# Kernel tuning notes

Hardware: AMD Instinct MI355X
Metric: run time of the kernel (lower is better)

The kernel has to match this reference:

```python
import jax, jax.numpy as jnp
import numpy as np

HID = 768  # hidden_size; feature dim is 2*HID


def setup_inputs() -> dict:
    key = jax.random.key(0)
    k1, k2 = jax.random.split(key)
    B, N, K, total_Q, D = 4, 10, 5, 512, 2 * HID
    support = jax.random.normal(k1, (B, N, K, D), dtype=jnp.float32)
    query = jax.random.normal(k2, (B, total_Q, D), dtype=jnp.float32)
    return {"support": support, "query": query, "N": N, "K": K, "total_Q": total_Q}


def reference(support, query, N, K, total_Q):
    B = support.shape[0]
    D = support.shape[-1]
    # (B, N*K, D)
    S = support.reshape(B, N * K, D)
    # negative squared euclidean distance: broadcast (B,1,NK,D) vs (B,Q,1,D) -> (B,Q,NK)
    dist_sq = -jnp.sum((S[:, None, :, :] - query[:, :, None, :]) ** 2, axis=3)
    dist_sq = dist_sq.reshape(B, total_Q, N, K)
    # query-guided weights: mean over queries, tanh, softmax over K -> (B,N,K,1)
    qgw = jax.nn.softmax(jnp.tanh(jnp.mean(dist_sq, axis=1)), axis=-1)[..., None]
    # weighted aggregation over shots -> (B,N,D)
    agg = jnp.sum(support * qgw, axis=2)
    return agg, qgw
```

## Files before the change

### kernel.cpp

```cpp
#include <hip/hip_runtime.h>
#include <math.h>

constexpr int B = 4;
constexpr int N = 10;
constexpr int K = 5;
constexpr int Q = 512;
constexpr int D = 1536;

constexpr int QBAR_OFF = 0;
constexpr int CSUM_OFF = B * D;

__global__ __launch_bounds__(256) void qstats_kernel(
    const float* __restrict__ query, float* __restrict__ ws) {
    const int tid = threadIdx.x;
    const int d   = blockIdx.y * 256 + tid;
    const int b   = blockIdx.z;
    const int q0  = blockIdx.x * 64;

    const float* qp = query + (size_t)b * Q * D + (size_t)q0 * D + d;
    float acc = 0.f, ssq = 0.f;
#pragma unroll 8
    for (int q = 0; q < 64; ++q) {
        float v = qp[(size_t)q * D];
        acc += v;
        ssq = fmaf(v, v, ssq);
    }
    atomicAdd(&ws[QBAR_OFF + b * D + d], acc);

    for (int off = 32; off > 0; off >>= 1) ssq += __shfl_down(ssq, off);
    __shared__ float red[4];
    const int wave = tid >> 6, lane = tid & 63;
    if (lane == 0) red[wave] = ssq;
    __syncthreads();
    if (tid == 0) {
        atomicAdd(&ws[CSUM_OFF + b], red[0] + red[1] + red[2] + red[3]);
    }
}

__global__ __launch_bounds__(256) void agg_kernel(
    const float* __restrict__ support, const float* __restrict__ ws,
    float* __restrict__ out) {
    const int tid = threadIdx.x;
    const int bn  = blockIdx.x;
    const int b   = bn / N;

    const float* sup  = support + (size_t)bn * K * D;
    const float* qbar = ws + QBAR_OFF + (size_t)b * D;

    __shared__ float s_red[2][K][4];
    __shared__ float s_w[K];

    const int wave = tid >> 6, lane = tid & 63;

    for (int k = 0; k < K; ++k) {
        float a = 0.f, c = 0.f;
        for (int d = tid; d < D; d += 256) {
            float s = sup[k * D + d];
            a = fmaf(s, s, a);
            c = fmaf(s, qbar[d], c);
        }
        for (int off = 32; off > 0; off >>= 1) {
            a += __shfl_down(a, off);
            c += __shfl_down(c, off);
        }
        if (lane == 0) { s_red[0][k][wave] = a; s_red[1][k][wave] = c; }
    }
    __syncthreads();

    if (tid < K) {
        const int k = tid;
        float ssk = s_red[0][k][0] + s_red[0][k][1] + s_red[0][k][2] + s_red[0][k][3];
        float sqk = s_red[1][k][0] + s_red[1][k][1] + s_red[1][k][2] + s_red[1][k][3];
        float cb  = ws[CSUM_OFF + b] * (1.f / Q);
        float m = -ssk + 2.f * sqk * (1.f / Q) - cb;
        s_w[k] = tanhf(m);
    }
    __syncthreads();
    if (tid == 0) {
        float mx = s_w[0];
        for (int k = 1; k < K; ++k) mx = fmaxf(mx, s_w[k]);
        float e[K], sum = 0.f;
        for (int k = 0; k < K; ++k) { e[k] = expf(s_w[k] - mx); sum += e[k]; }
        float inv = 1.f / sum;
        for (int k = 0; k < K; ++k) s_w[k] = e[k] * inv;
    }
    __syncthreads();

    if (tid < K) out[(size_t)B * N * D + bn * K + tid] = s_w[tid];

    float w[K];
#pragma unroll
    for (int k = 0; k < K; ++k) w[k] = s_w[k];

    for (int d = tid; d < D; d += 256) {
        float acc = 0.f;
#pragma unroll
        for (int k = 0; k < K; ++k) acc = fmaf(sup[k * D + d], w[k], acc);
        out[(size_t)bn * D + d] = acc;
    }
}

extern "C" void kernel_launch(void* const* d_in, const int* in_sizes, int n_in,
                              void* d_out, int out_size, void* d_ws, size_t ws_size,
                              hipStream_t stream) {
    const float* support = (const float*)d_in[0];
    const float* query   = (const float*)d_in[1];
    float* out = (float*)d_out;
    float* ws  = (float*)d_ws;

    hipMemsetAsync(d_ws, 0, (size_t)(B * D + B) * sizeof(float), stream);

    dim3 g1(Q / 64, D / 256, B);
    qstats_kernel<<<g1, 256, 0, stream>>>(query, ws);

    agg_kernel<<<B * N, 256, 0, stream>>>(support, ws, out);
}
```

Measured before the change: 86.51 us.

## Replace atomics and memset with partial-sum workspace reduced in agg kernel

The query-statistics kernel now writes per-chunk partial sums to distinct workspace slots instead of issuing atomicAdds. The aggregation kernel reduces those partials into shared memory (qbar and the squared-norm constant) before computing the weights. This removes the hipMemsetAsync launch and atomic contention, and the shared qbar also serves the dot-product loop. In exchange, each of the 40 agg blocks redundantly sums 8 partial rows of D floats.

```diff
diff --git a/kernel.cpp b/kernel.cpp
--- a/kernel.cpp
+++ b/kernel.cpp
@@ -7,17 +7,21 @@
 constexpr int Q = 512;
 constexpr int D = 1536;
 
-constexpr int QBAR_OFF = 0;
-constexpr int CSUM_OFF = B * D;
+constexpr int QCH = 8;
+constexpr int DCH = 6;
+
+constexpr int PART_OFF = 0;
+constexpr int CS_OFF   = QCH * B * D;
 
 __global__ __launch_bounds__(256) void qstats_kernel(
     const float* __restrict__ query, float* __restrict__ ws) {
     const int tid = threadIdx.x;
-    const int d   = blockIdx.y * 256 + tid;
+    const int c   = blockIdx.x;
+    const int y   = blockIdx.y;
     const int b   = blockIdx.z;
-    const int q0  = blockIdx.x * 64;
+    const int d   = y * 256 + tid;
 
-    const float* qp = query + (size_t)b * Q * D + (size_t)q0 * D + d;
+    const float* qp = query + (size_t)b * Q * D + (size_t)(c * 64) * D + d;
     float acc = 0.f, ssq = 0.f;
 #pragma unroll 8
     for (int q = 0; q < 64; ++q) {
@@ -25,7 +29,7 @@
         acc += v;
         ssq = fmaf(v, v, ssq);
     }
-    atomicAdd(&ws[QBAR_OFF + b * D + d], acc);
+    ws[PART_OFF + ((size_t)c * B + b) * D + d] = acc;
 
     for (int off = 32; off > 0; off >>= 1) ssq += __shfl_down(ssq, off);
     __shared__ float red[4];
@@ -33,7 +37,7 @@
     if (lane == 0) red[wave] = ssq;
     __syncthreads();
     if (tid == 0) {
-        atomicAdd(&ws[CSUM_OFF + b], red[0] + red[1] + red[2] + red[3]);
+        ws[CS_OFF + (b * QCH + c) * DCH + y] = red[0] + red[1] + red[2] + red[3];
     }
 }
 
@@ -44,26 +48,39 @@
     const int bn  = blockIdx.x;
     const int b   = bn / N;
 
-    const float* sup  = support + (size_t)bn * K * D;
-    const float* qbar = ws + QBAR_OFF + (size_t)b * D;
+    const float* sup = support + (size_t)bn * K * D;
 
+    __shared__ float s_qbar[D];
     __shared__ float s_red[2][K][4];
-    __shared__ float s_w[K];
+    __shared__ float s_w[K + 1];
+
+    for (int d = tid; d < D; d += 256) {
+        float s = 0.f;
+#pragma unroll
+        for (int c = 0; c < QCH; ++c)
+            s += ws[PART_OFF + ((size_t)c * B + b) * D + d];
+        s_qbar[d] = s;
+    }
+    if (tid < 64) {
+        float v = (tid < QCH * DCH) ? ws[CS_OFF + b * (QCH * DCH) + tid] : 0.f;
+        for (int off = 32; off > 0; off >>= 1) v += __shfl_down(v, off);
+        if (tid == 0) s_w[K] = v * (1.f / Q);
+    }
+    __syncthreads();
 
     const int wave = tid >> 6, lane = tid & 63;
-
     for (int k = 0; k < K; ++k) {
-        float a = 0.f, c = 0.f;
+        float a = 0.f, cdot = 0.f;
         for (int d = tid; d < D; d += 256) {
             float s = sup[k * D + d];
-            a = fmaf(s, s, a);
-            c = fmaf(s, qbar[d], c);
+            a    = fmaf(s, s, a);
+            cdot = fmaf(s, s_qbar[d], cdot);
         }
         for (int off = 32; off > 0; off >>= 1) {
-            a += __shfl_down(a, off);
-            c += __shfl_down(c, off);
+            a    += __shfl_down(a, off);
+            cdot += __shfl_down(cdot, off);
         }
-        if (lane == 0) { s_red[0][k][wave] = a; s_red[1][k][wave] = c; }
+        if (lane == 0) { s_red[0][k][wave] = a; s_red[1][k][wave] = cdot; }
     }
     __syncthreads();
 
@@ -71,8 +88,7 @@
         const int k = tid;
         float ssk = s_red[0][k][0] + s_red[0][k][1] + s_red[0][k][2] + s_red[0][k][3];
         float sqk = s_red[1][k][0] + s_red[1][k][1] + s_red[1][k][2] + s_red[1][k][3];
-        float cb  = ws[CSUM_OFF + b] * (1.f / Q);
-        float m = -ssk + 2.f * sqk * (1.f / Q) - cb;
+        float m = -ssk + 2.f * sqk * (1.f / Q) - s_w[K];
         s_w[k] = tanhf(m);
     }
     __syncthreads();
@@ -108,9 +124,7 @@
     float* out = (float*)d_out;
     float* ws  = (float*)d_ws;
 
-    hipMemsetAsync(d_ws, 0, (size_t)(B * D + B) * sizeof(float), stream);
-
-    dim3 g1(Q / 64, D / 256, B);
+    dim3 g1(QCH, DCH, B);
     qstats_kernel<<<g1, 256, 0, stream>>>(query, ws);
 
     agg_kernel<<<B * N, 256, 0, stream>>>(support, ws, out);
```

Measured after the change: 85.73 us. Within noise of the previous version (-0.9%).
